# Kernel optimization log

Hardware: AMD Instinct MI355X
Metric: run time of the kernel (lower is better)

Reference implementation:

```python
import math
import jax, jax.numpy as jnp
import numpy as np

N = 100000
E = 800000
IN_DIM = 128
HID = 128
HEADS = 4
C = HID // HEADS  # 32 per-head channels
TD = 16           # time encoding dim
NL = 2            # layers - 1 conv blocks
OUT = 2
BN_EPS = 1e-5


def setup_inputs() -> dict:
    key = jax.random.key(0)
    ks = jax.random.split(key, 24)
    s = 0.05
    inp = {
        "x": jax.random.normal(ks[0], (N, IN_DIM), dtype=jnp.float32),
        "edge_index": jax.random.randint(ks[1], (2, E), 0, N, dtype=jnp.int32),
        "timesteps": jax.random.randint(ks[2], (N,), 0, 100000, dtype=jnp.int32),
        # input projection Linear(in_dim + td, hid)
        "proj_w": jax.random.normal(ks[3], (IN_DIM + TD, HID), dtype=jnp.float32) * s,
        "proj_b": jnp.zeros((HID,), dtype=jnp.float32),
        # GATConv params per layer (stacked over NL layers)
        "conv_w": jax.random.normal(ks[4], (NL, HID, HID), dtype=jnp.float32) * s,
        "conv_b": jnp.zeros((NL, HID), dtype=jnp.float32),
        "att_src": jax.random.normal(ks[5], (NL, HEADS, C), dtype=jnp.float32) * s,
        "att_dst": jax.random.normal(ks[6], (NL, HEADS, C), dtype=jnp.float32) * s,
        # BatchNorm (eval mode: running stats)
        "bn_gamma": jax.random.uniform(ks[7], (NL, HID), dtype=jnp.float32) + 0.5,
        "bn_beta": jax.random.normal(ks[8], (NL, HID), dtype=jnp.float32) * s,
        "bn_mean": jax.random.normal(ks[9], (NL, HID), dtype=jnp.float32) * s,
        "bn_var": jax.random.uniform(ks[10], (NL, HID), dtype=jnp.float32) + 0.5,
        # age gate MLP: Linear(1,16) -> ReLU -> Linear(16,1) -> Sigmoid
        "gate_w1": jax.random.normal(ks[11], (1, 16), dtype=jnp.float32) * 0.5,
        "gate_b1": jnp.zeros((16,), dtype=jnp.float32),
        "gate_w2": jax.random.normal(ks[12], (16, 1), dtype=jnp.float32) * 0.5,
        "gate_b2": jnp.zeros((1,), dtype=jnp.float32),
        # head: Linear(hid, hid//2) -> ReLU -> Linear(hid//2, out)
        "head_w1": jax.random.normal(ks[13], (HID, HID // 2), dtype=jnp.float32) * s,
        "head_b1": jnp.zeros((HID // 2,), dtype=jnp.float32),
        "head_w2": jax.random.normal(ks[14], (HID // 2, OUT), dtype=jnp.float32) * s,
        "head_b2": jnp.zeros((OUT,), dtype=jnp.float32),
    }
    return inp


def _time_enc(t):
    # t: [N] float -> [N, TD] sinusoidal encoding
    t = t[:, None]
    freqs = jnp.exp(jnp.arange(0, TD, 2, dtype=jnp.float32) * (-(math.log(10000.0) / TD)))
    return jnp.concatenate([jnp.sin(t * freqs), jnp.cos(t * freqs)], axis=-1)


def _gat_conv(h_in, src, dst, W, b, a_src, a_dst):
    # h_in: [N, HID]; src/dst: [Etot] with self-loops included
    h = (h_in @ W).reshape(N, HEADS, C)                 # [N, H, C]
    al_s = jnp.sum(h * a_src[None], axis=-1)            # [N, H]
    al_d = jnp.sum(h * a_dst[None], axis=-1)            # [N, H]
    alpha = jax.nn.leaky_relu(al_s[src] + al_d[dst], 0.2)  # [Etot, H]
    # segment softmax over destination nodes
    m = jax.ops.segment_max(alpha, dst, num_segments=N)    # [N, H]
    ex = jnp.exp(alpha - m[dst])
    den = jax.ops.segment_sum(ex, dst, num_segments=N)     # [N, H]
    att = ex / (den[dst] + 1e-16)                          # [Etot, H]
    msg = h[src] * att[:, :, None]                         # [Etot, H, C]
    out = jax.ops.segment_sum(msg, dst, num_segments=N)    # [N, H, C]
    return out.reshape(N, HID) + b


def reference(x, edge_index, timesteps, proj_w, proj_b, conv_w, conv_b,
              att_src, att_dst, bn_gamma, bn_beta, bn_mean, bn_var,
              gate_w1, gate_b1, gate_w2, gate_b2,
              head_w1, head_b1, head_w2, head_b2):
    t = timesteps.astype(jnp.float32)
    te = _time_enc(t)                                      # [N, TD]
    h = jax.nn.relu(jnp.concatenate([x, te], axis=-1) @ proj_w + proj_b)
    # ages in [0, 1]
    mn, mx = jnp.min(t), jnp.max(t)
    ages = ((t - mn) / jnp.maximum(mx - mn, 1.0))[:, None]  # [N, 1]
    gate = jax.nn.sigmoid(jax.nn.relu(ages @ gate_w1 + gate_b1) @ gate_w2 + gate_b2)  # [N, 1]
    # add self-loops (PyG GATConv default)
    loop = jnp.arange(N, dtype=edge_index.dtype)
    src = jnp.concatenate([edge_index[0], loop])
    dst = jnp.concatenate([edge_index[1], loop])
    for i in range(NL):
        h = _gat_conv(h, src, dst, conv_w[i], conv_b[i], att_src[i], att_dst[i])
        h = (h - bn_mean[i]) * (bn_gamma[i] / jnp.sqrt(bn_var[i] + BN_EPS)) + bn_beta[i]
        h = jax.nn.elu(h)
        h = h * gate  # dropout is identity in eval mode
    h = jax.nn.relu(h @ head_w1 + head_b1)
    return h @ head_w2 + head_b2  # [N, OUT]
```

## Files before the change

### kernel.cpp

```cpp
#include <hip/hip_runtime.h>
#include <cfloat>
#include <climits>
#include <cmath>

constexpr int N_ = 100000;
constexpr int E_ = 800000;
constexpr int NBLK_ = (N_ + 255) / 256;

__global__ void k_init_minmax(int* minmax) {
    minmax[0] = INT_MAX;
    minmax[1] = INT_MIN;
}

__global__ __launch_bounds__(256) void k_prep(const int* __restrict__ ts, float* __restrict__ te,
                                              int* __restrict__ count, int* __restrict__ minmax) {
    const float FRQ[8] = {1.0f, 0.31622776601683794f, 0.1f, 0.031622776601683794f,
                          0.01f, 0.0031622776601683794f, 0.001f, 0.00031622776601683794f};
    int n = blockIdx.x * 256 + threadIdx.x;
    int tv_min = INT_MAX, tv_max = INT_MIN;
    if (n < N_) {
        int tv = ts[n];
        tv_min = tv; tv_max = tv;
        count[n] = 1;
        float tf = (float)tv;
#pragma unroll
        for (int j = 0; j < 8; ++j) {
            float ph = tf * FRQ[j];
            te[n * 16 + j] = sinf(ph);
            te[n * 16 + 8 + j] = cosf(ph);
        }
    }
#pragma unroll
    for (int o = 32; o >= 1; o >>= 1) {
        tv_min = min(tv_min, __shfl_xor(tv_min, o));
        tv_max = max(tv_max, __shfl_xor(tv_max, o));
    }
    if ((threadIdx.x & 63) == 0) {
        atomicMin(&minmax[0], tv_min);
        atomicMax(&minmax[1], tv_max);
    }
}

__global__ __launch_bounds__(256) void k_count(const int* __restrict__ ei, int* __restrict__ count) {
    int e = blockIdx.x * 256 + threadIdx.x;
    if (e < E_) atomicAdd(&count[ei[E_ + e]], 1);
}

__global__ __launch_bounds__(256) void k_bsum(const int* __restrict__ count, int* __restrict__ bsum) {
    int i = blockIdx.x * 256 + threadIdx.x;
    int v = (i < N_) ? count[i] : 0;
#pragma unroll
    for (int o = 32; o >= 1; o >>= 1) v += __shfl_xor(v, o);
    __shared__ int wsum[4];
    if ((threadIdx.x & 63) == 0) wsum[threadIdx.x >> 6] = v;
    __syncthreads();
    if (threadIdx.x == 0) bsum[blockIdx.x] = wsum[0] + wsum[1] + wsum[2] + wsum[3];
}

__global__ __launch_bounds__(512) void k_bscan(int* __restrict__ bsum, int* __restrict__ indptr) {
    int t = threadIdx.x;
    int v = (t < NBLK_) ? bsum[t] : 0;
    __shared__ int sc[512];
    sc[t] = v;
    __syncthreads();
    for (int o = 1; o < 512; o <<= 1) {
        int u = (t >= o) ? sc[t - o] : 0;
        __syncthreads();
        sc[t] += u;
        __syncthreads();
    }
    if (t < NBLK_) bsum[t] = sc[t] - v;
    if (t == NBLK_ - 1) indptr[N_] = sc[t];
}

__global__ __launch_bounds__(256) void k_scan_c(const int* __restrict__ count, const int* __restrict__ bsum,
                                                int* __restrict__ indptr, int* __restrict__ srcs,
                                                int* __restrict__ cursor) {
    int t = threadIdx.x;
    int i = blockIdx.x * 256 + t;
    int v = (i < N_) ? count[i] : 0;
    __shared__ int sc[256];
    sc[t] = v;
    __syncthreads();
    for (int o = 1; o < 256; o <<= 1) {
        int u = (t >= o) ? sc[t - o] : 0;
        __syncthreads();
        sc[t] += u;
        __syncthreads();
    }
    if (i < N_) {
        int off = bsum[blockIdx.x] + sc[t] - v;
        indptr[i] = off;
        srcs[off] = i;
        cursor[i] = off + 1;
    }
}

__global__ __launch_bounds__(256) void k_scatter(const int* __restrict__ ei, int* __restrict__ cursor,
                                                 int* __restrict__ srcs) {
    int e = blockIdx.x * 256 + threadIdx.x;
    if (e < E_) {
        int s = ei[e];
        int d = ei[E_ + e];
        int p = atomicAdd(&cursor[d], 1);
        srcs[p] = s;
    }
}

__global__ __launch_bounds__(256) void k_gate(const int* __restrict__ ts, const int* __restrict__ minmax,
                                              const float* __restrict__ gw1, const float* __restrict__ gb1,
                                              const float* __restrict__ gw2, const float* __restrict__ gb2,
                                              float* __restrict__ gate) {
    int n = blockIdx.x * 256 + threadIdx.x;
    if (n >= N_) return;
    float mn = (float)minmax[0], mx = (float)minmax[1];
    float age = ((float)ts[n] - mn) / fmaxf(mx - mn, 1.0f);
    float o = gb2[0];
#pragma unroll
    for (int j = 0; j < 16; ++j) {
        float hj = fmaxf(age * gw1[j] + gb1[j], 0.f);
        o += hj * gw2[j];
    }
    gate[n] = 1.f / (1.f + __expf(-o));
}

template <int K, int M, int MODE>
__global__ __launch_bounds__(256) void k_gemm(const float* __restrict__ A, const float* __restrict__ te,
                                              const float* __restrict__ W, const float* __restrict__ bias,
                                              const float* __restrict__ asrc, const float* __restrict__ adst,
                                              const float* __restrict__ w2, const float* __restrict__ b2,
                                              float* __restrict__ Cout, float* __restrict__ al_s,
                                              float* __restrict__ al_d) {
    constexpr int GR = 128, KC = 16;
    constexpr int NS = M / 64;
    __shared__ float As[KC][GR + 4];
    __shared__ float Ws[KC][M];
    __shared__ float asl[128], adl[128];
    __shared__ float w2l[128];
    const int r0 = blockIdx.x * GR;
    const int tid = threadIdx.x;
    const int tx = tid & 15, ty = tid >> 4;
    if (MODE == 1 && tid < 128) { asl[tid] = asrc[tid]; adl[tid] = adst[tid]; }
    if (MODE == 2 && tid < 128) { w2l[tid] = w2[tid]; }
    float acc[8][NS * 4];
#pragma unroll
    for (int i = 0; i < 8; ++i)
#pragma unroll
        for (int j = 0; j < NS * 4; ++j) acc[i][j] = 0.f;

    for (int k0 = 0; k0 < K; k0 += KC) {
        __syncthreads();
#pragma unroll
        for (int i = 0; i < 2; ++i) {
            int f = tid * 2 + i;
            int row = f >> 2, fq = f & 3;
            int gr = r0 + row;
            float4 v = make_float4(0.f, 0.f, 0.f, 0.f);
            if (gr < N_) {
                if (MODE == 0) {
                    if (k0 < 128) v = *(const float4*)&A[gr * 128 + k0 + fq * 4];
                    else          v = *(const float4*)&te[gr * 16 + fq * 4];
                } else {
                    v = *(const float4*)&A[gr * K + k0 + fq * 4];
                }
            }
            As[fq * 4 + 0][row] = v.x;
            As[fq * 4 + 1][row] = v.y;
            As[fq * 4 + 2][row] = v.z;
            As[fq * 4 + 3][row] = v.w;
        }
#pragma unroll
        for (int i = 0; i < (KC * M / 4) / 256; ++i) {
            int f = tid + i * 256;
            int kk = f / (M / 4), c4 = f % (M / 4);
            *(float4*)&Ws[kk][c4 * 4] = *(const float4*)&W[(k0 + kk) * M + c4 * 4];
        }
        __syncthreads();
#pragma unroll
        for (int kk = 0; kk < KC; ++kk) {
            float4 a0 = *(const float4*)&As[kk][ty * 8];
            float4 a1 = *(const float4*)&As[kk][ty * 8 + 4];
            float av[8] = {a0.x, a0.y, a0.z, a0.w, a1.x, a1.y, a1.z, a1.w};
            float wv[NS * 4];
#pragma unroll
            for (int s = 0; s < NS; ++s) {
                float4 w = *(const float4*)&Ws[kk][s * 64 + tx * 4];
                wv[s * 4 + 0] = w.x; wv[s * 4 + 1] = w.y;
                wv[s * 4 + 2] = w.z; wv[s * 4 + 3] = w.w;
            }
#pragma unroll
            for (int i = 0; i < 8; ++i)
#pragma unroll
                for (int j = 0; j < NS * 4; ++j) acc[i][j] = fmaf(av[i], wv[j], acc[i][j]);
        }
    }

#pragma unroll
    for (int i = 0; i < 8; ++i) {
        int gr = r0 + ty * 8 + i;
        bool valid = gr < N_;
        if (MODE == 0) {
            if (valid) {
#pragma unroll
                for (int s = 0; s < NS; ++s) {
                    float4 v;
                    v.x = fmaxf(acc[i][s * 4 + 0] + bias[s * 64 + tx * 4 + 0], 0.f);
                    v.y = fmaxf(acc[i][s * 4 + 1] + bias[s * 64 + tx * 4 + 1], 0.f);
                    v.z = fmaxf(acc[i][s * 4 + 2] + bias[s * 64 + tx * 4 + 2], 0.f);
                    v.w = fmaxf(acc[i][s * 4 + 3] + bias[s * 64 + tx * 4 + 3], 0.f);
                    *(float4*)&Cout[gr * M + s * 64 + tx * 4] = v;
                }
            }
        } else if (MODE == 1) {
            if (valid) {
#pragma unroll
                for (int s = 0; s < NS; ++s) {
                    float4 v = make_float4(acc[i][s * 4 + 0], acc[i][s * 4 + 1],
                                           acc[i][s * 4 + 2], acc[i][s * 4 + 3]);
                    *(float4*)&Cout[gr * M + s * 64 + tx * 4] = v;
                }
            }
#pragma unroll
            for (int s = 0; s < NS; ++s) {
                float ps = 0.f, pd = 0.f;
#pragma unroll
                for (int q = 0; q < 4; ++q) {
                    int c = s * 64 + tx * 4 + q;
                    ps = fmaf(acc[i][s * 4 + q], asl[c], ps);
                    pd = fmaf(acc[i][s * 4 + q], adl[c], pd);
                }
#pragma unroll
                for (int o = 1; o <= 4; o <<= 1) {
                    ps += __shfl_xor(ps, o);
                    pd += __shfl_xor(pd, o);
                }
                if (valid && (tx & 7) == 0) {
                    int head = 2 * s + (tx >> 3);
                    al_s[gr * 4 + head] = ps;
                    al_d[gr * 4 + head] = pd;
                }
            }
        } else {
            float ps0 = 0.f, ps1 = 0.f;
#pragma unroll
            for (int q = 0; q < 4; ++q) {
                float hv = fmaxf(acc[i][q] + bias[tx * 4 + q], 0.f);
                int c = tx * 4 + q;
                ps0 = fmaf(hv, w2l[c * 2 + 0], ps0);
                ps1 = fmaf(hv, w2l[c * 2 + 1], ps1);
            }
#pragma unroll
            for (int o = 1; o <= 8; o <<= 1) {
                ps0 += __shfl_xor(ps0, o);
                ps1 += __shfl_xor(ps1, o);
            }
            if (valid && tx == 0) {
                *(float2*)&Cout[gr * 2] = make_float2(ps0 + b2[0], ps1 + b2[1]);
            }
        }
    }
}

__global__ __launch_bounds__(256) void k_gat(const int* __restrict__ indptr, const int* __restrict__ srcs,
                                             const float* __restrict__ al_s, const float* __restrict__ al_d,
                                             const float* __restrict__ h2, const float* __restrict__ convb,
                                             const float* __restrict__ gamma, const float* __restrict__ beta,
                                             const float* __restrict__ mean, const float* __restrict__ var,
                                             const float* __restrict__ gate, float* __restrict__ hout) {
    int g = threadIdx.x >> 5, lg = threadIdx.x & 31;
    int n = blockIdx.x * 8 + g;
    if (n >= N_) return;
    int start = indptr[n], end = indptr[n + 1];
    int hl = lg >> 3;
    int c0 = lg * 4;
    float4 ad4 = *(const float4*)&al_d[n * 4];
    float adv[4] = {ad4.x, ad4.y, ad4.z, ad4.w};
    float M[4] = {-FLT_MAX, -FLT_MAX, -FLT_MAX, -FLT_MAX};
    float D[4] = {0.f, 0.f, 0.f, 0.f};
    float ac0 = 0.f, ac1 = 0.f, ac2 = 0.f, ac3 = 0.f;

    for (int p0 = start; p0 < end; p0 += 32) {
        int cs = end - p0;
        if (cs > 32) cs = 32;
        float a[4];
        int s = 0;
        if (lg < cs) {
            s = srcs[p0 + lg];
            float4 as4 = *(const float4*)&al_s[s * 4];
            float asv[4] = {as4.x, as4.y, as4.z, as4.w};
#pragma unroll
            for (int h = 0; h < 4; ++h) {
                float x = asv[h] + adv[h];
                a[h] = x > 0.f ? x : 0.2f * x;
            }
        } else {
#pragma unroll
            for (int h = 0; h < 4; ++h) a[h] = -FLT_MAX;
        }
        float f[4], w[4];
#pragma unroll
        for (int h = 0; h < 4; ++h) {
            float m = a[h];
#pragma unroll
            for (int o = 16; o >= 1; o >>= 1) m = fmaxf(m, __shfl_xor(m, o));
            float Mn = fmaxf(M[h], m);
            f[h] = __expf(M[h] - Mn);
            M[h] = Mn;
            w[h] = __expf(a[h] - Mn);
            float sv = w[h];
#pragma unroll
            for (int o = 16; o >= 1; o >>= 1) sv += __shfl_xor(sv, o);
            D[h] = D[h] * f[h] + sv;
        }
        float fh = hl < 2 ? (hl == 0 ? f[0] : f[1]) : (hl == 2 ? f[2] : f[3]);
        float whl = hl < 2 ? (hl == 0 ? w[0] : w[1]) : (hl == 2 ? w[2] : w[3]);
        ac0 *= fh; ac1 *= fh; ac2 *= fh; ac3 *= fh;
        int i = 0;
        for (; i + 1 < cs; i += 2) {
            float w0 = __shfl(whl, i, 32);
            float w1 = __shfl(whl, i + 1, 32);
            int s0 = __shfl(s, i, 32);
            int s1 = __shfl(s, i + 1, 32);
            float4 h0 = *(const float4*)&h2[s0 * 128 + c0];
            float4 h1 = *(const float4*)&h2[s1 * 128 + c0];
            ac0 = fmaf(w0, h0.x, ac0); ac1 = fmaf(w0, h0.y, ac1);
            ac2 = fmaf(w0, h0.z, ac2); ac3 = fmaf(w0, h0.w, ac3);
            ac0 = fmaf(w1, h1.x, ac0); ac1 = fmaf(w1, h1.y, ac1);
            ac2 = fmaf(w1, h1.z, ac2); ac3 = fmaf(w1, h1.w, ac3);
        }
        if (i < cs) {
            float w0 = __shfl(whl, i, 32);
            int s0 = __shfl(s, i, 32);
            float4 h0 = *(const float4*)&h2[s0 * 128 + c0];
            ac0 = fmaf(w0, h0.x, ac0); ac1 = fmaf(w0, h0.y, ac1);
            ac2 = fmaf(w0, h0.z, ac2); ac3 = fmaf(w0, h0.w, ac3);
        }
    }

    float Dh = hl < 2 ? (hl == 0 ? D[0] : D[1]) : (hl == 2 ? D[2] : D[3]);
    float rd = 1.0f / (Dh + 1e-16f);
    float gn = gate[n];
    float4 cb = *(const float4*)&convb[c0];
    float4 gm = *(const float4*)&gamma[c0];
    float4 bt = *(const float4*)&beta[c0];
    float4 mu = *(const float4*)&mean[c0];
    float4 vr = *(const float4*)&var[c0];
    float accs[4] = {ac0, ac1, ac2, ac3};
    float cbv[4] = {cb.x, cb.y, cb.z, cb.w};
    float gmv[4] = {gm.x, gm.y, gm.z, gm.w};
    float btv[4] = {bt.x, bt.y, bt.z, bt.w};
    float muv[4] = {mu.x, mu.y, mu.z, mu.w};
    float vrv[4] = {vr.x, vr.y, vr.z, vr.w};
    float4 outv;
    float* ov = (float*)&outv;
#pragma unroll
    for (int q = 0; q < 4; ++q) {
        float val = accs[q] * rd + cbv[q];
        float sc = gmv[q] * rsqrtf(vrv[q] + 1e-5f);
        val = (val - muv[q]) * sc + btv[q];
        val = val > 0.f ? val : expm1f(val);
        ov[q] = val * gn;
    }
    *(float4*)&hout[n * 128 + c0] = outv;
}

extern "C" void kernel_launch(void* const* d_in, const int* in_sizes, int n_in,
                              void* d_out, int out_size, void* d_ws, size_t ws_size,
                              hipStream_t stream) {
    const float* x       = (const float*)d_in[0];
    const int*   ei      = (const int*)d_in[1];
    const int*   ts      = (const int*)d_in[2];
    const float* proj_w  = (const float*)d_in[3];
    const float* proj_b  = (const float*)d_in[4];
    const float* conv_w  = (const float*)d_in[5];
    const float* conv_b  = (const float*)d_in[6];
    const float* att_src = (const float*)d_in[7];
    const float* att_dst = (const float*)d_in[8];
    const float* bn_g    = (const float*)d_in[9];
    const float* bn_b    = (const float*)d_in[10];
    const float* bn_m    = (const float*)d_in[11];
    const float* bn_v    = (const float*)d_in[12];
    const float* gw1     = (const float*)d_in[13];
    const float* gb1     = (const float*)d_in[14];
    const float* gw2     = (const float*)d_in[15];
    const float* gb2     = (const float*)d_in[16];
    const float* hw1     = (const float*)d_in[17];
    const float* hb1     = (const float*)d_in[18];
    const float* hw2     = (const float*)d_in[19];
    const float* hb2     = (const float*)d_in[20];
    float* out = (float*)d_out;

    float* ws   = (float*)d_ws;
    float* h    = ws;
    float* h2   = h + (size_t)N_ * 128;
    float* te   = h2 + (size_t)N_ * 128;
    float* al_s = te + (size_t)N_ * 16;
    float* al_d = al_s + (size_t)N_ * 4;
    float* gate = al_d + (size_t)N_ * 4;
    int* indptr = (int*)(gate + N_);
    int* srcs   = indptr + (N_ + 1);
    int* count  = srcs + (N_ + E_);
    int* cursor = count + N_;
    int* bsum   = cursor + N_;
    int* minmax = bsum + NBLK_ + 1;

    k_init_minmax<<<1, 1, 0, stream>>>(minmax);
    k_prep<<<(N_ + 255) / 256, 256, 0, stream>>>(ts, te, count, minmax);
    k_count<<<(E_ + 255) / 256, 256, 0, stream>>>(ei, count);
    k_bsum<<<NBLK_, 256, 0, stream>>>(count, bsum);
    k_bscan<<<1, 512, 0, stream>>>(bsum, indptr);
    k_scan_c<<<NBLK_, 256, 0, stream>>>(count, bsum, indptr, srcs, cursor);
    k_scatter<<<(E_ + 255) / 256, 256, 0, stream>>>(ei, cursor, srcs);
    k_gate<<<(N_ + 255) / 256, 256, 0, stream>>>(ts, minmax, gw1, gb1, gw2, gb2, gate);

    k_gemm<144, 128, 0><<<782, 256, 0, stream>>>(x, te, proj_w, proj_b, nullptr, nullptr,
                                                 nullptr, nullptr, h, nullptr, nullptr);
    for (int l = 0; l < 2; ++l) {
        k_gemm<128, 128, 1><<<782, 256, 0, stream>>>(h, nullptr, conv_w + l * 128 * 128, nullptr,
                                                     att_src + l * 128, att_dst + l * 128,
                                                     nullptr, nullptr, h2, al_s, al_d);
        k_gat<<<(N_ + 7) / 8, 256, 0, stream>>>(indptr, srcs, al_s, al_d, h2, conv_b + l * 128,
                                                bn_g + l * 128, bn_b + l * 128, bn_m + l * 128,
                                                bn_v + l * 128, gate, h);
    }
    k_gemm<128, 64, 2><<<782, 256, 0, stream>>>(h, nullptr, hw1, hb1, nullptr, nullptr,
                                                hw2, hb2, out, nullptr, nullptr);
}
```

Before: 510.1 us.

## Double-buffer GEMM tiles, narrow GAT node groups, fuse gate and minmax into prep kernels

The GEMM now prefetches the next K-chunk into registers while computing on the current shared-memory buffer, with two shared buffers and one barrier per chunk. The GAT aggregation uses 16 lanes per node with 8 channels each instead of 32 lanes with 4 channels, so each block handles twice as many nodes. The min/max reduction drops its global atomics and init kernel in favour of per-block partials reduced inside the block-scan kernel. The gate computation is folded into the scan kernel, and sin/cos become a single sincosf. Together these aim to hide load latency, cut kernel launches and raise per-lane work, at the cost of more shared memory and registers.

```diff
diff --git a/kernel.cpp b/kernel.cpp
--- a/kernel.cpp
+++ b/kernel.cpp
@@ -7,13 +7,9 @@
 constexpr int E_ = 800000;
 constexpr int NBLK_ = (N_ + 255) / 256;
 
-__global__ void k_init_minmax(int* minmax) {
-    minmax[0] = INT_MAX;
-    minmax[1] = INT_MIN;
-}
-
 __global__ __launch_bounds__(256) void k_prep(const int* __restrict__ ts, float* __restrict__ te,
-                                              int* __restrict__ count, int* __restrict__ minmax) {
+                                              int* __restrict__ count, int* __restrict__ bmin,
+                                              int* __restrict__ bmax) {
     const float FRQ[8] = {1.0f, 0.31622776601683794f, 0.1f, 0.031622776601683794f,
                           0.01f, 0.0031622776601683794f, 0.001f, 0.00031622776601683794f};
     int n = blockIdx.x * 256 + threadIdx.x;
@@ -25,9 +21,10 @@
         float tf = (float)tv;
 #pragma unroll
         for (int j = 0; j < 8; ++j) {
-            float ph = tf * FRQ[j];
-            te[n * 16 + j] = sinf(ph);
-            te[n * 16 + 8 + j] = cosf(ph);
+            float sv, cv;
+            sincosf(tf * FRQ[j], &sv, &cv);
+            te[n * 16 + j] = sv;
+            te[n * 16 + 8 + j] = cv;
         }
     }
 #pragma unroll
@@ -35,9 +32,15 @@
         tv_min = min(tv_min, __shfl_xor(tv_min, o));
         tv_max = max(tv_max, __shfl_xor(tv_max, o));
     }
+    __shared__ int smn[4], smx[4];
     if ((threadIdx.x & 63) == 0) {
-        atomicMin(&minmax[0], tv_min);
-        atomicMax(&minmax[1], tv_max);
+        smn[threadIdx.x >> 6] = tv_min;
+        smx[threadIdx.x >> 6] = tv_max;
+    }
+    __syncthreads();
+    if (threadIdx.x == 0) {
+        bmin[blockIdx.x] = min(min(smn[0], smn[1]), min(smn[2], smn[3]));
+        bmax[blockIdx.x] = max(max(smx[0], smx[1]), max(smx[2], smx[3]));
     }
 }
 
@@ -57,7 +60,9 @@
     if (threadIdx.x == 0) bsum[blockIdx.x] = wsum[0] + wsum[1] + wsum[2] + wsum[3];
 }
 
-__global__ __launch_bounds__(512) void k_bscan(int* __restrict__ bsum, int* __restrict__ indptr) {
+__global__ __launch_bounds__(512) void k_bscan(int* __restrict__ bsum, int* __restrict__ indptr,
+                                               const int* __restrict__ bmin, const int* __restrict__ bmax,
+                                               int* __restrict__ minmax) {
     int t = threadIdx.x;
     int v = (t < NBLK_) ? bsum[t] : 0;
     __shared__ int sc[512];
@@ -71,11 +76,31 @@
     }
     if (t < NBLK_) bsum[t] = sc[t] - v;
     if (t == NBLK_ - 1) indptr[N_] = sc[t];
+    int mn = (t < NBLK_) ? bmin[t] : INT_MAX;
+    int mx = (t < NBLK_) ? bmax[t] : INT_MIN;
+#pragma unroll
+    for (int o = 32; o >= 1; o >>= 1) {
+        mn = min(mn, __shfl_xor(mn, o));
+        mx = max(mx, __shfl_xor(mx, o));
+    }
+    __shared__ int rmn[8], rmx[8];
+    if ((t & 63) == 0) { rmn[t >> 6] = mn; rmx[t >> 6] = mx; }
+    __syncthreads();
+    if (t == 0) {
+        int a = INT_MAX, b = INT_MIN;
+#pragma unroll
+        for (int q = 0; q < 8; ++q) { a = min(a, rmn[q]); b = max(b, rmx[q]); }
+        minmax[0] = a;
+        minmax[1] = b;
+    }
 }
 
 __global__ __launch_bounds__(256) void k_scan_c(const int* __restrict__ count, const int* __restrict__ bsum,
                                                 int* __restrict__ indptr, int* __restrict__ srcs,
-                                                int* __restrict__ cursor) {
+                                                int* __restrict__ cursor, const int* __restrict__ ts,
+                                                const int* __restrict__ minmax, const float* __restrict__ gw1,
+                                                const float* __restrict__ gb1, const float* __restrict__ gw2,
+                                                const float* __restrict__ gb2, float* __restrict__ gate) {
     int t = threadIdx.x;
     int i = blockIdx.x * 256 + t;
     int v = (i < N_) ? count[i] : 0;
@@ -93,6 +118,15 @@
         indptr[i] = off;
         srcs[off] = i;
         cursor[i] = off + 1;
+        float mn = (float)minmax[0], mx = (float)minmax[1];
+        float age = ((float)ts[i] - mn) / fmaxf(mx - mn, 1.0f);
+        float o2 = gb2[0];
+#pragma unroll
+        for (int j = 0; j < 16; ++j) {
+            float hj = fmaxf(age * gw1[j] + gb1[j], 0.f);
+            o2 += hj * gw2[j];
+        }
+        gate[i] = 1.f / (1.f + __expf(-o2));
     }
 }
 
@@ -105,23 +139,6 @@
         int p = atomicAdd(&cursor[d], 1);
         srcs[p] = s;
     }
-}
-
-__global__ __launch_bounds__(256) void k_gate(const int* __restrict__ ts, const int* __restrict__ minmax,
-                                              const float* __restrict__ gw1, const float* __restrict__ gb1,
-                                              const float* __restrict__ gw2, const float* __restrict__ gb2,
-                                              float* __restrict__ gate) {
-    int n = blockIdx.x * 256 + threadIdx.x;
-    if (n >= N_) return;
-    float mn = (float)minmax[0], mx = (float)minmax[1];
-    float age = ((float)ts[n] - mn) / fmaxf(mx - mn, 1.0f);
-    float o = gb2[0];
-#pragma unroll
-    for (int j = 0; j < 16; ++j) {
-        float hj = fmaxf(age * gw1[j] + gb1[j], 0.f);
-        o += hj * gw2[j];
-    }
-    gate[n] = 1.f / (1.f + __expf(-o));
 }
 
 template <int K, int M, int MODE>
@@ -133,8 +150,10 @@
                                               float* __restrict__ al_d) {
     constexpr int GR = 128, KC = 16;
     constexpr int NS = M / 64;
-    __shared__ float As[KC][GR + 4];
-    __shared__ float Ws[KC][M];
+    constexpr int NCH = (K + KC - 1) / KC;
+    constexpr int NW = KC * M / 1024;
+    __shared__ float As[2][KC][GR + 4];
+    __shared__ float Ws[2][KC][M];
     __shared__ float asl[128], adl[128];
     __shared__ float w2l[128];
     const int r0 = blockIdx.x * GR;
@@ -148,43 +167,65 @@
 #pragma unroll
         for (int j = 0; j < NS * 4; ++j) acc[i][j] = 0.f;
 
-    for (int k0 = 0; k0 < K; k0 += KC) {
-        __syncthreads();
+    float4 ra[2], rw[NW];
+    const int arow = (tid * 2) >> 2;
+    const int agr = r0 + arow;
+
+    auto ldg = [&](int c) {
+        int k0 = c * KC;
 #pragma unroll
         for (int i = 0; i < 2; ++i) {
-            int f = tid * 2 + i;
-            int row = f >> 2, fq = f & 3;
-            int gr = r0 + row;
+            int fq = (tid * 2 + i) & 3;
             float4 v = make_float4(0.f, 0.f, 0.f, 0.f);
-            if (gr < N_) {
+            if (agr < N_) {
                 if (MODE == 0) {
-                    if (k0 < 128) v = *(const float4*)&A[gr * 128 + k0 + fq * 4];
-                    else          v = *(const float4*)&te[gr * 16 + fq * 4];
+                    if (k0 < 128) v = *(const float4*)&A[agr * 128 + k0 + fq * 4];
+                    else          v = *(const float4*)&te[agr * 16 + fq * 4];
                 } else {
-                    v = *(const float4*)&A[gr * K + k0 + fq * 4];
-                }
-            }
-            As[fq * 4 + 0][row] = v.x;
-            As[fq * 4 + 1][row] = v.y;
-            As[fq * 4 + 2][row] = v.z;
-            As[fq * 4 + 3][row] = v.w;
-        }
-#pragma unroll
-        for (int i = 0; i < (KC * M / 4) / 256; ++i) {
+                    v = *(const float4*)&A[agr * K + k0 + fq * 4];
+                }
+            }
+            ra[i] = v;
+        }
+#pragma unroll
+        for (int i = 0; i < NW; ++i) {
             int f = tid + i * 256;
             int kk = f / (M / 4), c4 = f % (M / 4);
-            *(float4*)&Ws[kk][c4 * 4] = *(const float4*)&W[(k0 + kk) * M + c4 * 4];
-        }
-        __syncthreads();
+            rw[i] = *(const float4*)&W[(k0 + kk) * M + c4 * 4];
+        }
+    };
+    auto sts = [&](int b) {
+#pragma unroll
+        for (int i = 0; i < 2; ++i) {
+            int fq = (tid * 2 + i) & 3;
+            As[b][fq * 4 + 0][arow] = ra[i].x;
+            As[b][fq * 4 + 1][arow] = ra[i].y;
+            As[b][fq * 4 + 2][arow] = ra[i].z;
+            As[b][fq * 4 + 3][arow] = ra[i].w;
+        }
+#pragma unroll
+        for (int i = 0; i < NW; ++i) {
+            int f = tid + i * 256;
+            int kk = f / (M / 4), c4 = f % (M / 4);
+            *(float4*)&Ws[b][kk][c4 * 4] = rw[i];
+        }
+    };
+
+    ldg(0);
+    sts(0);
+    __syncthreads();
+    for (int c = 0; c < NCH; ++c) {
+        const int cur = c & 1;
+        if (c + 1 < NCH) ldg(c + 1);
 #pragma unroll
         for (int kk = 0; kk < KC; ++kk) {
-            float4 a0 = *(const float4*)&As[kk][ty * 8];
-            float4 a1 = *(const float4*)&As[kk][ty * 8 + 4];
+            float4 a0 = *(const float4*)&As[cur][kk][ty * 8];
+            float4 a1 = *(const float4*)&As[cur][kk][ty * 8 + 4];
             float av[8] = {a0.x, a0.y, a0.z, a0.w, a1.x, a1.y, a1.z, a1.w};
             float wv[NS * 4];
 #pragma unroll
             for (int s = 0; s < NS; ++s) {
-                float4 w = *(const float4*)&Ws[kk][s * 64 + tx * 4];
+                float4 w = *(const float4*)&Ws[cur][kk][s * 64 + tx * 4];
                 wv[s * 4 + 0] = w.x; wv[s * 4 + 1] = w.y;
                 wv[s * 4 + 2] = w.z; wv[s * 4 + 3] = w.w;
             }
@@ -192,6 +233,10 @@
             for (int i = 0; i < 8; ++i)
 #pragma unroll
                 for (int j = 0; j < NS * 4; ++j) acc[i][j] = fmaf(av[i], wv[j], acc[i][j]);
+        }
+        if (c + 1 < NCH) {
+            sts(cur ^ 1);
+            __syncthreads();
         }
     }
 
@@ -267,21 +312,22 @@
                                              const float* __restrict__ gamma, const float* __restrict__ beta,
                                              const float* __restrict__ mean, const float* __restrict__ var,
                                              const float* __restrict__ gate, float* __restrict__ hout) {
-    int g = threadIdx.x >> 5, lg = threadIdx.x & 31;
-    int n = blockIdx.x * 8 + g;
+    int g = threadIdx.x >> 4, lg = threadIdx.x & 15;
+    int n = blockIdx.x * 16 + g;
     if (n >= N_) return;
     int start = indptr[n], end = indptr[n + 1];
-    int hl = lg >> 3;
-    int c0 = lg * 4;
+    int hl = lg >> 2;
+    int c0 = lg * 8;
+    float gn = gate[n];
     float4 ad4 = *(const float4*)&al_d[n * 4];
     float adv[4] = {ad4.x, ad4.y, ad4.z, ad4.w};
     float M[4] = {-FLT_MAX, -FLT_MAX, -FLT_MAX, -FLT_MAX};
     float D[4] = {0.f, 0.f, 0.f, 0.f};
-    float ac0 = 0.f, ac1 = 0.f, ac2 = 0.f, ac3 = 0.f;
-
-    for (int p0 = start; p0 < end; p0 += 32) {
+    float ac[8] = {0.f, 0.f, 0.f, 0.f, 0.f, 0.f, 0.f, 0.f};
+
+    for (int p0 = start; p0 < end; p0 += 16) {
         int cs = end - p0;
-        if (cs > 32) cs = 32;
+        if (cs > 16) cs = 16;
         float a[4];
         int s = 0;
         if (lg < cs) {
@@ -302,66 +348,78 @@
         for (int h = 0; h < 4; ++h) {
             float m = a[h];
 #pragma unroll
-            for (int o = 16; o >= 1; o >>= 1) m = fmaxf(m, __shfl_xor(m, o));
+            for (int o = 8; o >= 1; o >>= 1) m = fmaxf(m, __shfl_xor(m, o));
             float Mn = fmaxf(M[h], m);
             f[h] = __expf(M[h] - Mn);
             M[h] = Mn;
             w[h] = __expf(a[h] - Mn);
             float sv = w[h];
 #pragma unroll
-            for (int o = 16; o >= 1; o >>= 1) sv += __shfl_xor(sv, o);
+            for (int o = 8; o >= 1; o >>= 1) sv += __shfl_xor(sv, o);
             D[h] = D[h] * f[h] + sv;
         }
         float fh = hl < 2 ? (hl == 0 ? f[0] : f[1]) : (hl == 2 ? f[2] : f[3]);
         float whl = hl < 2 ? (hl == 0 ? w[0] : w[1]) : (hl == 2 ? w[2] : w[3]);
-        ac0 *= fh; ac1 *= fh; ac2 *= fh; ac3 *= fh;
+#pragma unroll
+        for (int q = 0; q < 8; ++q) ac[q] *= fh;
         int i = 0;
         for (; i + 1 < cs; i += 2) {
-            float w0 = __shfl(whl, i, 32);
-            float w1 = __shfl(whl, i + 1, 32);
-            int s0 = __shfl(s, i, 32);
-            int s1 = __shfl(s, i + 1, 32);
-            float4 h0 = *(const float4*)&h2[s0 * 128 + c0];
-            float4 h1 = *(const float4*)&h2[s1 * 128 + c0];
-            ac0 = fmaf(w0, h0.x, ac0); ac1 = fmaf(w0, h0.y, ac1);
-            ac2 = fmaf(w0, h0.z, ac2); ac3 = fmaf(w0, h0.w, ac3);
-            ac0 = fmaf(w1, h1.x, ac0); ac1 = fmaf(w1, h1.y, ac1);
-            ac2 = fmaf(w1, h1.z, ac2); ac3 = fmaf(w1, h1.w, ac3);
+            float w0 = __shfl(whl, i, 16);
+            float w1 = __shfl(whl, i + 1, 16);
+            int s0 = __shfl(s, i, 16);
+            int s1 = __shfl(s, i + 1, 16);
+            float4 h0a = *(const float4*)&h2[s0 * 128 + c0];
+            float4 h0b = *(const float4*)&h2[s0 * 128 + c0 + 4];
+            float4 h1a = *(const float4*)&h2[s1 * 128 + c0];
+            float4 h1b = *(const float4*)&h2[s1 * 128 + c0 + 4];
+            ac[0] = fmaf(w0, h0a.x, ac[0]); ac[1] = fmaf(w0, h0a.y, ac[1]);
+            ac[2] = fmaf(w0, h0a.z, ac[2]); ac[3] = fmaf(w0, h0a.w, ac[3]);
+            ac[4] = fmaf(w0, h0b.x, ac[4]); ac[5] = fmaf(w0, h0b.y, ac[5]);
+            ac[6] = fmaf(w0, h0b.z, ac[6]); ac[7] = fmaf(w0, h0b.w, ac[7]);
+            ac[0] = fmaf(w1, h1a.x, ac[0]); ac[1] = fmaf(w1, h1a.y, ac[1]);
+            ac[2] = fmaf(w1, h1a.z, ac[2]); ac[3] = fmaf(w1, h1a.w, ac[3]);
+            ac[4] = fmaf(w1, h1b.x, ac[4]); ac[5] = fmaf(w1, h1b.y, ac[5]);
+            ac[6] = fmaf(w1, h1b.z, ac[6]); ac[7] = fmaf(w1, h1b.w, ac[7]);
         }
         if (i < cs) {
-            float w0 = __shfl(whl, i, 32);
-            int s0 = __shfl(s, i, 32);
-            float4 h0 = *(const float4*)&h2[s0 * 128 + c0];
-            ac0 = fmaf(w0, h0.x, ac0); ac1 = fmaf(w0, h0.y, ac1);
-            ac2 = fmaf(w0, h0.z, ac2); ac3 = fmaf(w0, h0.w, ac3);
+            float w0 = __shfl(whl, i, 16);
+            int s0 = __shfl(s, i, 16);
+            float4 h0a = *(const float4*)&h2[s0 * 128 + c0];
+            float4 h0b = *(const float4*)&h2[s0 * 128 + c0 + 4];
+            ac[0] = fmaf(w0, h0a.x, ac[0]); ac[1] = fmaf(w0, h0a.y, ac[1]);
+            ac[2] = fmaf(w0, h0a.z, ac[2]); ac[3] = fmaf(w0, h0a.w, ac[3]);
+            ac[4] = fmaf(w0, h0b.x, ac[4]); ac[5] = fmaf(w0, h0b.y, ac[5]);
+            ac[6] = fmaf(w0, h0b.z, ac[6]); ac[7] = fmaf(w0, h0b.w, ac[7]);
         }
     }
 
     float Dh = hl < 2 ? (hl == 0 ? D[0] : D[1]) : (hl == 2 ? D[2] : D[3]);
     float rd = 1.0f / (Dh + 1e-16f);
-    float gn = gate[n];
-    float4 cb = *(const float4*)&convb[c0];
-    float4 gm = *(const float4*)&gamma[c0];
-    float4 bt = *(const float4*)&beta[c0];
-    float4 mu = *(const float4*)&mean[c0];
-    float4 vr = *(const float4*)&var[c0];
-    float accs[4] = {ac0, ac1, ac2, ac3};
-    float cbv[4] = {cb.x, cb.y, cb.z, cb.w};
-    float gmv[4] = {gm.x, gm.y, gm.z, gm.w};
-    float btv[4] = {bt.x, bt.y, bt.z, bt.w};
-    float muv[4] = {mu.x, mu.y, mu.z, mu.w};
-    float vrv[4] = {vr.x, vr.y, vr.z, vr.w};
-    float4 outv;
-    float* ov = (float*)&outv;
-#pragma unroll
-    for (int q = 0; q < 4; ++q) {
-        float val = accs[q] * rd + cbv[q];
-        float sc = gmv[q] * rsqrtf(vrv[q] + 1e-5f);
-        val = (val - muv[q]) * sc + btv[q];
-        val = val > 0.f ? val : expm1f(val);
-        ov[q] = val * gn;
-    }
-    *(float4*)&hout[n * 128 + c0] = outv;
+    float out8[8];
+#pragma unroll
+    for (int half = 0; half < 2; ++half) {
+        int cb0 = c0 + half * 4;
+        float4 cb = *(const float4*)&convb[cb0];
+        float4 gm = *(const float4*)&gamma[cb0];
+        float4 bt = *(const float4*)&beta[cb0];
+        float4 mu = *(const float4*)&mean[cb0];
+        float4 vr = *(const float4*)&var[cb0];
+        float cbv[4] = {cb.x, cb.y, cb.z, cb.w};
+        float gmv[4] = {gm.x, gm.y, gm.z, gm.w};
+        float btv[4] = {bt.x, bt.y, bt.z, bt.w};
+        float muv[4] = {mu.x, mu.y, mu.z, mu.w};
+        float vrv[4] = {vr.x, vr.y, vr.z, vr.w};
+#pragma unroll
+        for (int q = 0; q < 4; ++q) {
+            float val = ac[half * 4 + q] * rd + cbv[q];
+            float sc = gmv[q] * rsqrtf(vrv[q] + 1e-5f);
+            val = (val - muv[q]) * sc + btv[q];
+            val = val > 0.f ? val : expm1f(val);
+            out8[half * 4 + q] = val * gn;
+        }
+    }
+    *(float4*)&hout[n * 128 + c0] = make_float4(out8[0], out8[1], out8[2], out8[3]);
+    *(float4*)&hout[n * 128 + c0 + 4] = make_float4(out8[4], out8[5], out8[6], out8[7]);
 }
 
 extern "C" void kernel_launch(void* const* d_in, const int* in_sizes, int n_in,
@@ -402,16 +460,17 @@
     int* count  = srcs + (N_ + E_);
     int* cursor = count + N_;
     int* bsum   = cursor + N_;
-    int* minmax = bsum + NBLK_ + 1;
-
-    k_init_minmax<<<1, 1, 0, stream>>>(minmax);
-    k_prep<<<(N_ + 255) / 256, 256, 0, stream>>>(ts, te, count, minmax);
+    int* bmin   = bsum + NBLK_;
+    int* bmax   = bmin + NBLK_;
+    int* minmax = bmax + NBLK_;
+
+    k_prep<<<NBLK_, 256, 0, stream>>>(ts, te, count, bmin, bmax);
     k_count<<<(E_ + 255) / 256, 256, 0, stream>>>(ei, count);
     k_bsum<<<NBLK_, 256, 0, stream>>>(count, bsum);
-    k_bscan<<<1, 512, 0, stream>>>(bsum, indptr);
-    k_scan_c<<<NBLK_, 256, 0, stream>>>(count, bsum, indptr, srcs, cursor);
+    k_bscan<<<1, 512, 0, stream>>>(bsum, indptr, bmin, bmax, minmax);
+    k_scan_c<<<NBLK_, 256, 0, stream>>>(count, bsum, indptr, srcs, cursor, ts, minmax,
+                                        gw1, gb1, gw2, gb2, gate);
     k_scatter<<<(E_ + 255) / 256, 256, 0, stream>>>(ei, cursor, srcs);
-    k_gate<<<(N_ + 255) / 256, 256, 0, stream>>>(ts, minmax, gw1, gb1, gw2, gb2, gate);
 
     k_gemm<144, 128, 0><<<782, 256, 0, stream>>>(x, te, proj_w, proj_b, nullptr, nullptr,
                                                  nullptr, nullptr, h, nullptr, nullptr);
@@ -419,9 +478,9 @@
         k_gemm<128, 128, 1><<<782, 256, 0, stream>>>(h, nullptr, conv_w + l * 128 * 128, nullptr,
                                                      att_src + l * 128, att_dst + l * 128,
                                                      nullptr, nullptr, h2, al_s, al_d);
-        k_gat<<<(N_ + 7) / 8, 256, 0, stream>>>(indptr, srcs, al_s, al_d, h2, conv_b + l * 128,
-                                                bn_g + l * 128, bn_b + l * 128, bn_m + l * 128,
-                                                bn_v + l * 128, gate, h);
+        k_gat<<<(N_ + 15) / 16, 256, 0, stream>>>(indptr, srcs, al_s, al_d, h2, conv_b + l * 128,
+                                                  bn_g + l * 128, bn_b + l * 128, bn_m + l * 128,
+                                                  bn_v + l * 128, gate, h);
     }
     k_gemm<128, 64, 2><<<782, 256, 0, stream>>>(h, nullptr, hw1, hb1, nullptr, nullptr,
                                                 hw2, hb2, out, nullptr, nullptr);
```

New measurement: 595.3 us. 16.7% more time.
